# Performance work log

Hardware: AMD Instinct MI355X
Metric: run time of the kernel (lower is better)

Reference implementation:

```python
import jax, jax.numpy as jnp
import numpy as np

B, T, H, N, IN, W, D = 4096, 128, 64, 16, 32, 128, 8


def lipswish(x):
    return 0.909 * jax.nn.silu(x)


def setup_inputs() -> dict:
    key = jax.random.key(0)
    ks = jax.random.split(key, 10)

    def lin(k, i, o):
        kw, kb = jax.random.split(k)
        w = jax.random.normal(kw, (i, o), jnp.float32) / np.sqrt(i).astype(np.float32)
        b = jax.random.normal(kb, (o,), jnp.float32) * 0.01
        return w, b

    init_w0, init_b0 = lin(ks[0], IN, W)
    init_w1, init_b1 = lin(ks[1], W, H)
    drift_w0, drift_b0 = lin(ks[2], H + 1, W)
    drift_w1, drift_b1 = lin(ks[3], W, H)
    diff_w0, diff_b0 = lin(ks[4], H + 1, W)
    diff_w1, diff_b1 = lin(ks[5], W, H * N)
    ro_w, ro_b = lin(ks[6], H, D)
    ts = jnp.arange(T, dtype=jnp.float32)
    init_noise = jax.random.normal(ks[7], (B, IN), jnp.float32)
    # Brownian increments for unit steps: dW ~ N(0, dt) with dt = 1.
    dW = jax.random.normal(ks[8], (B, T - 1, N), jnp.float32)
    return dict(ts=ts, init_noise=init_noise, dW=dW,
                init_w0=init_w0, init_b0=init_b0, init_w1=init_w1, init_b1=init_b1,
                drift_w0=drift_w0, drift_b0=drift_b0, drift_w1=drift_w1, drift_b1=drift_b1,
                diff_w0=diff_w0, diff_b0=diff_b0, diff_w1=diff_w1, diff_b1=diff_b1,
                ro_w=ro_w, ro_b=ro_b)


def reference(ts, init_noise, dW,
              init_w0, init_b0, init_w1, init_b1,
              drift_w0, drift_b0, drift_w1, drift_b1,
              diff_w0, diff_b0, diff_w1, diff_b1,
              ro_w, ro_b):
    # initial MLP: default relu activation, identity final activation
    y0 = jnp.maximum(init_noise @ init_w0 + init_b0, 0.0) @ init_w1 + init_b1  # [B, H]

    def with_t(t, y):
        return jnp.concatenate([jnp.full((y.shape[0], 1), t, y.dtype), y], axis=1)

    def drift(t, y):  # [B, H]
        h = lipswish(with_t(t, y) @ drift_w0 + drift_b0)
        return jnp.tanh(h @ drift_w1 + drift_b1)

    def diffusion(t, y):  # [B, H, N]
        h = lipswish(with_t(t, y) @ diff_w0 + diff_b0)
        g = jnp.tanh(h @ diff_w1 + diff_b1)
        return g.reshape(y.shape[0], H, N)

    f0 = drift(ts[0], y0)
    g0 = diffusion(ts[0], y0)

    def step(carry, inp):
        y, yhat, f, g = carry
        t0, t1, dw = inp  # dw: [B, N]
        dt = t1 - t0
        # ReversibleHeun: yhat1 = 2 y - yhat + (f dt + g dW)
        yhat1 = 2.0 * y - yhat + f * dt + jnp.einsum('bhn,bn->bh', g, dw)
        f1 = drift(t1, yhat1)
        g1 = diffusion(t1, yhat1)
        y1 = y + 0.5 * ((f + f1) * dt + jnp.einsum('bhn,bn->bh', g + g1, dw))
        return (y1, yhat1, f1, g1), y1

    dWs = jnp.swapaxes(dW, 0, 1)  # [T-1, B, N]
    _, ys = jax.lax.scan(step, (y0, y0, f0, g0), (ts[:-1], ts[1:], dWs))
    ys = jnp.concatenate([y0[None], ys], axis=0)  # [T, B, H]
    out = jnp.einsum('tbh,hd->tbd', ys, ro_w) + ro_b
    return jnp.swapaxes(out, 0, 1)  # [B, T, D]
```

## Files before the change

### kernel.cpp

```cpp
#include <hip/hip_runtime.h>

#define NTHREADS 512
#define BB 8
#define SP 68


struct alignas(16) SMem {
    float dw0[65 * 128];
    float gw0[65 * 128];
    float db0[128];
    float db1[64];
    float gb0[128];
    float ro[512];
    float rob[8];
    float y[BB * SP];
    float yh[BB * SP];
    float f[BB * SP];
    float h[BB * 128];
    float dwn[BB * 16];
};

__device__ __forceinline__ float lipswish_f(float x) {
    const float e = expf(-x);
    const float d = __fadd_rn(1.0f, e);
    const float t = __fmul_rn(0.909f, x);
    return __fdiv_rn(t, d);
}

__global__ __launch_bounds__(NTHREADS, 4)
void sde_kernel(const float* __restrict__ ts, const float* __restrict__ init_noise,
                const float* __restrict__ dWin,
                const float* __restrict__ iw0, const float* __restrict__ ib0,
                const float* __restrict__ iw1, const float* __restrict__ ib1,
                const float* __restrict__ dr_w0, const float* __restrict__ dr_b0,
                const float* __restrict__ dr_w1, const float* __restrict__ dr_b1,
                const float* __restrict__ di_w0, const float* __restrict__ di_b0,
                const float* __restrict__ di_w1, const float* __restrict__ di_b1,
                const float* __restrict__ ro_w, const float* __restrict__ ro_b,
                float* __restrict__ out)
{
    __shared__ SMem sm;
    const int tid  = threadIdx.x;
    const int lane = tid & 63;
    const int wv   = tid >> 6;
    const int cg   = wv & 3;
    const int rg   = wv >> 2;
    const int b0   = blockIdx.x * BB;
    const int c0   = cg * 256 + (lane << 2);

    for (int i = tid; i < 65 * 128; i += NTHREADS) {
        sm.dw0[i] = dr_w0[i];
        sm.gw0[i] = di_w0[i];
    }
    if (tid < 128) sm.db0[tid] = dr_b0[tid];
    if (tid < 64)  sm.db1[tid] = dr_b1[tid];
    if (tid < 128) sm.gb0[tid] = di_b0[tid];
    if (tid < 512) sm.ro[tid] = ro_w[tid];
    if (tid < 8) sm.rob[tid] = ro_b[tid];

    float gb1v[4];
    {
        const float4 bv = *(const float4*)&di_b1[c0];
        gb1v[0] = bv.x; gb1v[1] = bv.y; gb1v[2] = bv.z; gb1v[3] = bv.w;
    }

    for (int i = tid; i < BB * 32; i += NTHREADS)
        sm.f[i] = init_noise[(size_t)(b0 + (i >> 5)) * 32 + (i & 31)];
    __syncthreads();

    {
        const int j = tid & 127, bq = tid >> 7;
        float acc[2];
        const float bj = ib0[j];
#pragma unroll
        for (int bi = 0; bi < 2; ++bi) acc[bi] = bj;
        for (int i = 0; i < 32; ++i) {
            const float w = iw0[i * 128 + j];
#pragma unroll
            for (int bi = 0; bi < 2; ++bi)
                acc[bi] = __fmaf_rn(sm.f[(bq * 2 + bi) * 32 + i], w, acc[bi]);
        }
#pragma unroll
        for (int bi = 0; bi < 2; ++bi)
            sm.h[(bq * 2 + bi) * 128 + j] = fmaxf(acc[bi], 0.0f);
    }
    __syncthreads();
    {
        const int hh = tid & 63, bg = tid >> 6;
        float acc = ib1[hh];
        for (int k = 0; k < 128; ++k)
            acc = __fmaf_rn(sm.h[bg * 128 + k], iw1[k * 64 + hh], acc);
        sm.y[bg * SP + hh]  = acc;
        sm.yh[bg * SP + hh] = acc;
    }
    __syncthreads();

    auto readout = [&](int trow) {
        if (tid < 64) {
            const int b = tid >> 3, d = tid & 7;
            float acc = sm.rob[d];
#pragma unroll
            for (int hh = 0; hh < 64; ++hh)
                acc = __fmaf_rn(sm.y[b * SP + hh], sm.ro[hh * 8 + d], acc);
            out[((size_t)(b0 + b) * 128 + trow) * 8 + d] = acc;
        }
    };
    readout(0);

    float g[4][4];

    auto layer1 = [&](const float* w0s, const float* b0s, float t1f) {
        const int j = tid & 127, bq = tid >> 7;
        float acc[2];
        const float bj = b0s[j];
        const float wt = w0s[j];
#pragma unroll
        for (int bi = 0; bi < 2; ++bi) acc[bi] = __fmaf_rn(t1f, wt, bj);
#pragma unroll 4
        for (int i = 0; i < 64; i += 4) {
            const float w0_ = w0s[(1 + i) * 128 + j];
            const float w1_ = w0s[(2 + i) * 128 + j];
            const float w2_ = w0s[(3 + i) * 128 + j];
            const float w3_ = w0s[(4 + i) * 128 + j];
#pragma unroll
            for (int bi = 0; bi < 2; ++bi) {
                const float4 xv = *(const float4*)&sm.yh[(bq * 2 + bi) * SP + i];
                acc[bi] = __fmaf_rn(xv.x, w0_, acc[bi]);
                acc[bi] = __fmaf_rn(xv.y, w1_, acc[bi]);
                acc[bi] = __fmaf_rn(xv.z, w2_, acc[bi]);
                acc[bi] = __fmaf_rn(xv.w, w3_, acc[bi]);
            }
        }
#pragma unroll
        for (int bi = 0; bi < 2; ++bi)
            sm.h[(bq * 2 + bi) * 128 + j] = lipswish_f(acc[bi]);
    };

    auto ein_bfly = [&](const float v[4], int b) -> float {
        float part = 0.0f;
#pragma unroll
        for (int e = 0; e < 4; ++e)
            part = __fmaf_rn(v[e], sm.dwn[b * 16 + (lane & 3) * 4 + e], part);
        part = __fadd_rn(part, __shfl_xor(part, 1, 64));
        part = __fadd_rn(part, __shfl_xor(part, 2, 64));
        return part;
    };

    auto mlp = [&](float t1f, float dtf, bool upd) {
        layer1(sm.dw0, sm.db0, t1f);
        __syncthreads();
        {
            const int hh = tid & 63, bg = tid >> 6;
            float acc = sm.db1[hh];
#pragma unroll 4
            for (int k = 0; k < 128; ++k)
                acc = __fmaf_rn(sm.h[bg * 128 + k], dr_w1[k * 64 + hh], acc);
            sm.f[bg * SP + hh] = tanhf(acc);
        }
        __syncthreads();
        layer1(sm.gw0, sm.gb0, t1f);
        __syncthreads();
        {
            float acc[4][4];
#pragma unroll
            for (int bi = 0; bi < 4; ++bi)
#pragma unroll
                for (int e = 0; e < 4; ++e) acc[bi][e] = 0.0f;

            float4 wA[4], wB[4], hA[4], hB[4];
#pragma unroll
            for (int t = 0; t < 4; ++t)
                wA[t] = *(const float4*)&di_w1[(size_t)t * 1024 + c0];
#pragma unroll
            for (int bi = 0; bi < 4; ++bi)
                hA[bi] = *(const float4*)&sm.h[(rg * 4 + bi) * 128];

#pragma unroll 1
            for (int kb = 0; kb < 128; kb += 8) {
                const int k2 = kb + 4;
#pragma unroll
                for (int t = 0; t < 4; ++t)
                    wB[t] = *(const float4*)&di_w1[(size_t)(k2 + t) * 1024 + c0];
#pragma unroll
                for (int bi = 0; bi < 4; ++bi)
                    hB[bi] = *(const float4*)&sm.h[(rg * 4 + bi) * 128 + k2];
#pragma unroll
                for (int bi = 0; bi < 4; ++bi) {
                    acc[bi][0] = __fmaf_rn(hA[bi].x, wA[0].x, acc[bi][0]);
                    acc[bi][1] = __fmaf_rn(hA[bi].x, wA[0].y, acc[bi][1]);
                    acc[bi][2] = __fmaf_rn(hA[bi].x, wA[0].z, acc[bi][2]);
                    acc[bi][3] = __fmaf_rn(hA[bi].x, wA[0].w, acc[bi][3]);
                    acc[bi][0] = __fmaf_rn(hA[bi].y, wA[1].x, acc[bi][0]);
                    acc[bi][1] = __fmaf_rn(hA[bi].y, wA[1].y, acc[bi][1]);
                    acc[bi][2] = __fmaf_rn(hA[bi].y, wA[1].z, acc[bi][2]);
                    acc[bi][3] = __fmaf_rn(hA[bi].y, wA[1].w, acc[bi][3]);
                    acc[bi][0] = __fmaf_rn(hA[bi].z, wA[2].x, acc[bi][0]);
                    acc[bi][1] = __fmaf_rn(hA[bi].z, wA[2].y, acc[bi][1]);
                    acc[bi][2] = __fmaf_rn(hA[bi].z, wA[2].z, acc[bi][2]);
                    acc[bi][3] = __fmaf_rn(hA[bi].z, wA[2].w, acc[bi][3]);
                    acc[bi][0] = __fmaf_rn(hA[bi].w, wA[3].x, acc[bi][0]);
                    acc[bi][1] = __fmaf_rn(hA[bi].w, wA[3].y, acc[bi][1]);
                    acc[bi][2] = __fmaf_rn(hA[bi].w, wA[3].z, acc[bi][2]);
                    acc[bi][3] = __fmaf_rn(hA[bi].w, wA[3].w, acc[bi][3]);
                }
                const int k3 = (kb + 8) & 127;
#pragma unroll
                for (int t = 0; t < 4; ++t)
                    wA[t] = *(const float4*)&di_w1[(size_t)(k3 + t) * 1024 + c0];
#pragma unroll
                for (int bi = 0; bi < 4; ++bi)
                    hA[bi] = *(const float4*)&sm.h[(rg * 4 + bi) * 128 + k3];
#pragma unroll
                for (int bi = 0; bi < 4; ++bi) {
                    acc[bi][0] = __fmaf_rn(hB[bi].x, wB[0].x, acc[bi][0]);
                    acc[bi][1] = __fmaf_rn(hB[bi].x, wB[0].y, acc[bi][1]);
                    acc[bi][2] = __fmaf_rn(hB[bi].x, wB[0].z, acc[bi][2]);
                    acc[bi][3] = __fmaf_rn(hB[bi].x, wB[0].w, acc[bi][3]);
                    acc[bi][0] = __fmaf_rn(hB[bi].y, wB[1].x, acc[bi][0]);
                    acc[bi][1] = __fmaf_rn(hB[bi].y, wB[1].y, acc[bi][1]);
                    acc[bi][2] = __fmaf_rn(hB[bi].y, wB[1].z, acc[bi][2]);
                    acc[bi][3] = __fmaf_rn(hB[bi].y, wB[1].w, acc[bi][3]);
                    acc[bi][0] = __fmaf_rn(hB[bi].z, wB[2].x, acc[bi][0]);
                    acc[bi][1] = __fmaf_rn(hB[bi].z, wB[2].y, acc[bi][1]);
                    acc[bi][2] = __fmaf_rn(hB[bi].z, wB[2].z, acc[bi][2]);
                    acc[bi][3] = __fmaf_rn(hB[bi].z, wB[2].w, acc[bi][3]);
                    acc[bi][0] = __fmaf_rn(hB[bi].w, wB[3].x, acc[bi][0]);
                    acc[bi][1] = __fmaf_rn(hB[bi].w, wB[3].y, acc[bi][1]);
                    acc[bi][2] = __fmaf_rn(hB[bi].w, wB[3].z, acc[bi][2]);
                    acc[bi][3] = __fmaf_rn(hB[bi].w, wB[3].w, acc[bi][3]);
                }
            }

#pragma unroll
            for (int bi = 0; bi < 4; ++bi) {
                const int b = rg * 4 + bi;
                float gv4[4];
#pragma unroll
                for (int e = 0; e < 4; ++e) {
                    const float gv = tanhf(__fadd_rn(acc[bi][e], gb1v[e]));
                    gv4[e] = gv;
                    g[bi][e] = gv;
                }
                if (upd) {
                    const float ein2 = ein_bfly(gv4, b);
                    if ((lane & 3) == 0) {
                        const int hh  = cg * 16 + (lane >> 2);
                        const int idx = b * SP + hh;
                        const float tot = __fmaf_rn(dtf, sm.f[idx], ein2);
                        sm.y[idx] = __fmaf_rn(0.5f, tot, sm.y[idx]);
                    }
                }
            }
        }
        __syncthreads();
    };

    mlp(ts[0], 0.0f, false);

    for (int s = 0; s < 127; ++s) {
        const float t1f = ts[s + 1];
        const float dtf = __fsub_rn(t1f, ts[s]);

        if (tid < BB * 16)
            sm.dwn[tid] = dWin[((size_t)(b0 + (tid >> 4)) * 127 + s) * 16 + (tid & 15)];
        __syncthreads();

#pragma unroll
        for (int bi = 0; bi < 4; ++bi) {
            const int b = rg * 4 + bi;
            const float ein1 = ein_bfly(g[bi], b);
            if ((lane & 3) == 0) {
                const int hh  = cg * 16 + (lane >> 2);
                const int idx = b * SP + hh;
                const float yv  = sm.y[idx];
                const float yhv = sm.yh[idx];
                const float inc = __fmaf_rn(dtf, sm.f[idx], ein1);
                const float a1  = __fmaf_rn(2.0f, yv, -yhv);
                sm.yh[idx] = __fadd_rn(a1, inc);
                sm.y[idx]  = __fmaf_rn(0.5f, inc, yv);
            }
        }
        __syncthreads();

        mlp(t1f, dtf, true);
        readout(s + 1);
    }
}

extern "C" void kernel_launch(void* const* d_in, const int* in_sizes, int n_in,
                              void* d_out, int out_size, void* d_ws, size_t ws_size,
                              hipStream_t stream) {
    (void)in_sizes; (void)n_in; (void)d_ws; (void)ws_size; (void)out_size;
    const float* ts         = (const float*)d_in[0];
    const float* init_noise = (const float*)d_in[1];
    const float* dW         = (const float*)d_in[2];
    const float* iw0        = (const float*)d_in[3];
    const float* ib0        = (const float*)d_in[4];
    const float* iw1        = (const float*)d_in[5];
    const float* ib1        = (const float*)d_in[6];
    const float* dr_w0      = (const float*)d_in[7];
    const float* dr_b0      = (const float*)d_in[8];
    const float* dr_w1      = (const float*)d_in[9];
    const float* dr_b1      = (const float*)d_in[10];
    const float* di_w0      = (const float*)d_in[11];
    const float* di_b0      = (const float*)d_in[12];
    const float* di_w1      = (const float*)d_in[13];
    const float* di_b1      = (const float*)d_in[14];
    const float* ro_w       = (const float*)d_in[15];
    const float* ro_b       = (const float*)d_in[16];
    float* out = (float*)d_out;

    sde_kernel<<<dim3(4096 / BB), dim3(NTHREADS), 0, stream>>>(
        ts, init_noise, dW, iw0, ib0, iw1, ib1,
        dr_w0, dr_b0, dr_w1, dr_b1, di_w0, di_b0, di_w1, di_b1,
        ro_w, ro_b, out);
}
```

Baseline: 3.745 ms.

## Fuse drift and diffusion MLP layers, keep state in registers, cut barriers

Computes the drift and diffusion first layers in one pass over yhat, and folds the drift second layer into the diffusion second-layer GEMM loop. Per-thread state (y, yhat, f, midpoint) now lives in registers, and f is shared within each 4-lane group by shuffles. dW is prefetched one step ahead into registers instead of staged through shared memory. This cuts the barriers per step from about six to three and removes the separate f and readout shared buffers. In exchange, register pressure rises at 4 blocks per CU, and the readout now reads weights straight from global memory.

```diff
diff --git a/kernel.cpp b/kernel.cpp
--- a/kernel.cpp
+++ b/kernel.cpp
@@ -11,13 +11,10 @@
     float db0[128];
     float db1[64];
     float gb0[128];
-    float ro[512];
-    float rob[8];
-    float y[BB * SP];
+    float y [BB * SP];
     float yh[BB * SP];
-    float f[BB * SP];
-    float h[BB * 128];
-    float dwn[BB * 16];
+    float hd[BB * 128];
+    float hg[BB * 128];
 };
 
 __device__ __forceinline__ float lipswish_f(float x) {
@@ -47,6 +44,10 @@
     const int rg   = wv >> 2;
     const int b0   = blockIdx.x * BB;
     const int c0   = cg * 256 + (lane << 2);
+    const int q    = lane & 3;
+    const int hh_own = cg * 16 + (lane >> 2);
+    const int rb   = rg * 4 + q;
+    const bool owner = (q == 0);
 
     for (int i = tid; i < 65 * 128; i += NTHREADS) {
         sm.dw0[i] = dr_w0[i];
@@ -55,8 +56,6 @@
     if (tid < 128) sm.db0[tid] = dr_b0[tid];
     if (tid < 64)  sm.db1[tid] = dr_b1[tid];
     if (tid < 128) sm.gb0[tid] = di_b0[tid];
-    if (tid < 512) sm.ro[tid] = ro_w[tid];
-    if (tid < 8) sm.rob[tid] = ro_b[tid];
 
     float gb1v[4];
     {
@@ -65,7 +64,7 @@
     }
 
     for (int i = tid; i < BB * 32; i += NTHREADS)
-        sm.f[i] = init_noise[(size_t)(b0 + (i >> 5)) * 32 + (i & 31)];
+        sm.hg[i] = init_noise[(size_t)(b0 + (i >> 5)) * 32 + (i & 31)];
     __syncthreads();
 
     {
@@ -78,213 +77,248 @@
             const float w = iw0[i * 128 + j];
 #pragma unroll
             for (int bi = 0; bi < 2; ++bi)
-                acc[bi] = __fmaf_rn(sm.f[(bq * 2 + bi) * 32 + i], w, acc[bi]);
+                acc[bi] = __fmaf_rn(sm.hg[(bq * 2 + bi) * 32 + i], w, acc[bi]);
         }
 #pragma unroll
         for (int bi = 0; bi < 2; ++bi)
-            sm.h[(bq * 2 + bi) * 128 + j] = fmaxf(acc[bi], 0.0f);
+            sm.hd[(bq * 2 + bi) * 128 + j] = fmaxf(acc[bi], 0.0f);
     }
     __syncthreads();
     {
         const int hh = tid & 63, bg = tid >> 6;
         float acc = ib1[hh];
         for (int k = 0; k < 128; ++k)
-            acc = __fmaf_rn(sm.h[bg * 128 + k], iw1[k * 64 + hh], acc);
+            acc = __fmaf_rn(sm.hd[bg * 128 + k], iw1[k * 64 + hh], acc);
         sm.y[bg * SP + hh]  = acc;
         sm.yh[bg * SP + hh] = acc;
     }
     __syncthreads();
 
     auto readout = [&](int trow) {
-        if (tid < 64) {
-            const int b = tid >> 3, d = tid & 7;
-            float acc = sm.rob[d];
-#pragma unroll
-            for (int hh = 0; hh < 64; ++hh)
-                acc = __fmaf_rn(sm.y[b * SP + hh], sm.ro[hh * 8 + d], acc);
-            out[((size_t)(b0 + b) * 128 + trow) * 8 + d] = acc;
-        }
+        const int b = tid >> 3, d = tid & 7;
+        float acc = ro_b[d];
+#pragma unroll
+        for (int hh = 0; hh < 64; ++hh)
+            acc = __fmaf_rn(sm.y[b * SP + hh], ro_w[hh * 8 + d], acc);
+        out[((size_t)(b0 + b) * 128 + trow) * 8 + d] = acc;
     };
-    readout(0);
-
+
+    float y4[4], yh4[4], ymid4[4], f4[4];
     float g[4][4];
-
-    auto layer1 = [&](const float* w0s, const float* b0s, float t1f) {
-        const int j = tid & 127, bq = tid >> 7;
-        float acc[2];
-        const float bj = b0s[j];
-        const float wt = w0s[j];
-#pragma unroll
-        for (int bi = 0; bi < 2; ++bi) acc[bi] = __fmaf_rn(t1f, wt, bj);
-#pragma unroll 4
-        for (int i = 0; i < 64; i += 4) {
-            const float w0_ = w0s[(1 + i) * 128 + j];
-            const float w1_ = w0s[(2 + i) * 128 + j];
-            const float w2_ = w0s[(3 + i) * 128 + j];
-            const float w3_ = w0s[(4 + i) * 128 + j];
-#pragma unroll
-            for (int bi = 0; bi < 2; ++bi) {
-                const float4 xv = *(const float4*)&sm.yh[(bq * 2 + bi) * SP + i];
-                acc[bi] = __fmaf_rn(xv.x, w0_, acc[bi]);
-                acc[bi] = __fmaf_rn(xv.y, w1_, acc[bi]);
-                acc[bi] = __fmaf_rn(xv.z, w2_, acc[bi]);
-                acc[bi] = __fmaf_rn(xv.w, w3_, acc[bi]);
-            }
-        }
-#pragma unroll
-        for (int bi = 0; bi < 2; ++bi)
-            sm.h[(bq * 2 + bi) * 128 + j] = lipswish_f(acc[bi]);
-    };
-
-    auto ein_bfly = [&](const float v[4], int b) -> float {
+    float4 dwC[4], dwN[4];
+
+#pragma unroll
+    for (int bi = 0; bi < 4; ++bi) {
+        const float v = sm.y[(rg * 4 + bi) * SP + hh_own];
+        y4[bi] = v; yh4[bi] = v;
+        dwC[bi] = *(const float4*)&dWin[((size_t)(b0 + rg * 4 + bi) * 127 + 0) * 16 + q * 4];
+        ymid4[bi] = 0.0f; f4[bi] = 0.0f;
+    }
+
+    auto ein_bfly = [&](const float v[4], const float4 dw) -> float {
         float part = 0.0f;
-#pragma unroll
-        for (int e = 0; e < 4; ++e)
-            part = __fmaf_rn(v[e], sm.dwn[b * 16 + (lane & 3) * 4 + e], part);
+        part = __fmaf_rn(v[0], dw.x, part);
+        part = __fmaf_rn(v[1], dw.y, part);
+        part = __fmaf_rn(v[2], dw.z, part);
+        part = __fmaf_rn(v[3], dw.w, part);
         part = __fadd_rn(part, __shfl_xor(part, 1, 64));
         part = __fadd_rn(part, __shfl_xor(part, 2, 64));
         return part;
     };
 
-    auto mlp = [&](float t1f, float dtf, bool upd) {
-        layer1(sm.dw0, sm.db0, t1f);
-        __syncthreads();
+    auto layer12 = [&](float t1f) {
+        const int j = tid & 127, bq = tid >> 7;
+        float aD[2], aG[2];
         {
-            const int hh = tid & 63, bg = tid >> 6;
-            float acc = sm.db1[hh];
+            const float bD = sm.db0[j], wtD = sm.dw0[j];
+            const float bG = sm.gb0[j], wtG = sm.gw0[j];
+#pragma unroll
+            for (int bi = 0; bi < 2; ++bi) {
+                aD[bi] = __fmaf_rn(t1f, wtD, bD);
+                aG[bi] = __fmaf_rn(t1f, wtG, bG);
+            }
+        }
 #pragma unroll 4
-            for (int k = 0; k < 128; ++k)
-                acc = __fmaf_rn(sm.h[bg * 128 + k], dr_w1[k * 64 + hh], acc);
-            sm.f[bg * SP + hh] = tanhf(acc);
-        }
-        __syncthreads();
-        layer1(sm.gw0, sm.gb0, t1f);
-        __syncthreads();
-        {
-            float acc[4][4];
+        for (int i = 0; i < 64; i += 4) {
+            const float wD0 = sm.dw0[(1 + i) * 128 + j];
+            const float wD1 = sm.dw0[(2 + i) * 128 + j];
+            const float wD2 = sm.dw0[(3 + i) * 128 + j];
+            const float wD3 = sm.dw0[(4 + i) * 128 + j];
+            const float wG0 = sm.gw0[(1 + i) * 128 + j];
+            const float wG1 = sm.gw0[(2 + i) * 128 + j];
+            const float wG2 = sm.gw0[(3 + i) * 128 + j];
+            const float wG3 = sm.gw0[(4 + i) * 128 + j];
+#pragma unroll
+            for (int bi = 0; bi < 2; ++bi) {
+                const float4 xv = *(const float4*)&sm.yh[(bq * 2 + bi) * SP + i];
+                aD[bi] = __fmaf_rn(xv.x, wD0, aD[bi]);
+                aD[bi] = __fmaf_rn(xv.y, wD1, aD[bi]);
+                aD[bi] = __fmaf_rn(xv.z, wD2, aD[bi]);
+                aD[bi] = __fmaf_rn(xv.w, wD3, aD[bi]);
+                aG[bi] = __fmaf_rn(xv.x, wG0, aG[bi]);
+                aG[bi] = __fmaf_rn(xv.y, wG1, aG[bi]);
+                aG[bi] = __fmaf_rn(xv.z, wG2, aG[bi]);
+                aG[bi] = __fmaf_rn(xv.w, wG3, aG[bi]);
+            }
+        }
+#pragma unroll
+        for (int bi = 0; bi < 2; ++bi) {
+            sm.hd[(bq * 2 + bi) * 128 + j] = lipswish_f(aD[bi]);
+            sm.hg[(bq * 2 + bi) * 128 + j] = lipswish_f(aG[bi]);
+        }
+    };
+
+    auto gf_phase = [&](float dtf, bool upd) {
+        float acc[4][4];
+#pragma unroll
+        for (int bi = 0; bi < 4; ++bi)
+#pragma unroll
+            for (int e = 0; e < 4; ++e) acc[bi][e] = 0.0f;
+        float fa = sm.db1[hh_own];
+
+        float4 wA[4], wB[4], hA[4], hB[4];
+#pragma unroll
+        for (int t = 0; t < 4; ++t)
+            wA[t] = *(const float4*)&di_w1[(size_t)t * 1024 + c0];
+#pragma unroll
+        for (int bi = 0; bi < 4; ++bi)
+            hA[bi] = *(const float4*)&sm.hg[(rg * 4 + bi) * 128];
+
+#pragma unroll 1
+        for (int kb = 0; kb < 128; kb += 8) {
+            const int k2 = kb + 4;
+            const float fw0 = dr_w1[(kb + 0) * 64 + hh_own];
+            const float fw1 = dr_w1[(kb + 1) * 64 + hh_own];
+            const float fw2 = dr_w1[(kb + 2) * 64 + hh_own];
+            const float fw3 = dr_w1[(kb + 3) * 64 + hh_own];
+            const float fw4 = dr_w1[(kb + 4) * 64 + hh_own];
+            const float fw5 = dr_w1[(kb + 5) * 64 + hh_own];
+            const float fw6 = dr_w1[(kb + 6) * 64 + hh_own];
+            const float fw7 = dr_w1[(kb + 7) * 64 + hh_own];
+#pragma unroll
+            for (int t = 0; t < 4; ++t)
+                wB[t] = *(const float4*)&di_w1[(size_t)(k2 + t) * 1024 + c0];
 #pragma unroll
             for (int bi = 0; bi < 4; ++bi)
-#pragma unroll
-                for (int e = 0; e < 4; ++e) acc[bi][e] = 0.0f;
-
-            float4 wA[4], wB[4], hA[4], hB[4];
+                hB[bi] = *(const float4*)&sm.hg[(rg * 4 + bi) * 128 + k2];
+#pragma unroll
+            for (int bi = 0; bi < 4; ++bi) {
+                acc[bi][0] = __fmaf_rn(hA[bi].x, wA[0].x, acc[bi][0]);
+                acc[bi][1] = __fmaf_rn(hA[bi].x, wA[0].y, acc[bi][1]);
+                acc[bi][2] = __fmaf_rn(hA[bi].x, wA[0].z, acc[bi][2]);
+                acc[bi][3] = __fmaf_rn(hA[bi].x, wA[0].w, acc[bi][3]);
+                acc[bi][0] = __fmaf_rn(hA[bi].y, wA[1].x, acc[bi][0]);
+                acc[bi][1] = __fmaf_rn(hA[bi].y, wA[1].y, acc[bi][1]);
+                acc[bi][2] = __fmaf_rn(hA[bi].y, wA[1].z, acc[bi][2]);
+                acc[bi][3] = __fmaf_rn(hA[bi].y, wA[1].w, acc[bi][3]);
+                acc[bi][0] = __fmaf_rn(hA[bi].z, wA[2].x, acc[bi][0]);
+                acc[bi][1] = __fmaf_rn(hA[bi].z, wA[2].y, acc[bi][1]);
+                acc[bi][2] = __fmaf_rn(hA[bi].z, wA[2].z, acc[bi][2]);
+                acc[bi][3] = __fmaf_rn(hA[bi].z, wA[2].w, acc[bi][3]);
+                acc[bi][0] = __fmaf_rn(hA[bi].w, wA[3].x, acc[bi][0]);
+                acc[bi][1] = __fmaf_rn(hA[bi].w, wA[3].y, acc[bi][1]);
+                acc[bi][2] = __fmaf_rn(hA[bi].w, wA[3].z, acc[bi][2]);
+                acc[bi][3] = __fmaf_rn(hA[bi].w, wA[3].w, acc[bi][3]);
+            }
+            const int k3 = (kb + 8) & 127;
 #pragma unroll
             for (int t = 0; t < 4; ++t)
-                wA[t] = *(const float4*)&di_w1[(size_t)t * 1024 + c0];
+                wA[t] = *(const float4*)&di_w1[(size_t)(k3 + t) * 1024 + c0];
 #pragma unroll
             for (int bi = 0; bi < 4; ++bi)
-                hA[bi] = *(const float4*)&sm.h[(rg * 4 + bi) * 128];
-
-#pragma unroll 1
-            for (int kb = 0; kb < 128; kb += 8) {
-                const int k2 = kb + 4;
-#pragma unroll
-                for (int t = 0; t < 4; ++t)
-                    wB[t] = *(const float4*)&di_w1[(size_t)(k2 + t) * 1024 + c0];
-#pragma unroll
-                for (int bi = 0; bi < 4; ++bi)
-                    hB[bi] = *(const float4*)&sm.h[(rg * 4 + bi) * 128 + k2];
-#pragma unroll
-                for (int bi = 0; bi < 4; ++bi) {
-                    acc[bi][0] = __fmaf_rn(hA[bi].x, wA[0].x, acc[bi][0]);
-                    acc[bi][1] = __fmaf_rn(hA[bi].x, wA[0].y, acc[bi][1]);
-                    acc[bi][2] = __fmaf_rn(hA[bi].x, wA[0].z, acc[bi][2]);
-                    acc[bi][3] = __fmaf_rn(hA[bi].x, wA[0].w, acc[bi][3]);
-                    acc[bi][0] = __fmaf_rn(hA[bi].y, wA[1].x, acc[bi][0]);
-                    acc[bi][1] = __fmaf_rn(hA[bi].y, wA[1].y, acc[bi][1]);
-                    acc[bi][2] = __fmaf_rn(hA[bi].y, wA[1].z, acc[bi][2]);
-                    acc[bi][3] = __fmaf_rn(hA[bi].y, wA[1].w, acc[bi][3]);
-                    acc[bi][0] = __fmaf_rn(hA[bi].z, wA[2].x, acc[bi][0]);
-                    acc[bi][1] = __fmaf_rn(hA[bi].z, wA[2].y, acc[bi][1]);
-                    acc[bi][2] = __fmaf_rn(hA[bi].z, wA[2].z, acc[bi][2]);
-                    acc[bi][3] = __fmaf_rn(hA[bi].z, wA[2].w, acc[bi][3]);
-                    acc[bi][0] = __fmaf_rn(hA[bi].w, wA[3].x, acc[bi][0]);
-                    acc[bi][1] = __fmaf_rn(hA[bi].w, wA[3].y, acc[bi][1]);
-                    acc[bi][2] = __fmaf_rn(hA[bi].w, wA[3].z, acc[bi][2]);
-                    acc[bi][3] = __fmaf_rn(hA[bi].w, wA[3].w, acc[bi][3]);
+                hA[bi] = *(const float4*)&sm.hg[(rg * 4 + bi) * 128 + k3];
+#pragma unroll
+            for (int bi = 0; bi < 4; ++bi) {
+                acc[bi][0] = __fmaf_rn(hB[bi].x, wB[0].x, acc[bi][0]);
+                acc[bi][1] = __fmaf_rn(hB[bi].x, wB[0].y, acc[bi][1]);
+                acc[bi][2] = __fmaf_rn(hB[bi].x, wB[0].z, acc[bi][2]);
+                acc[bi][3] = __fmaf_rn(hB[bi].x, wB[0].w, acc[bi][3]);
+                acc[bi][0] = __fmaf_rn(hB[bi].y, wB[1].x, acc[bi][0]);
+                acc[bi][1] = __fmaf_rn(hB[bi].y, wB[1].y, acc[bi][1]);
+                acc[bi][2] = __fmaf_rn(hB[bi].y, wB[1].z, acc[bi][2]);
+                acc[bi][3] = __fmaf_rn(hB[bi].y, wB[1].w, acc[bi][3]);
+                acc[bi][0] = __fmaf_rn(hB[bi].z, wB[2].x, acc[bi][0]);
+                acc[bi][1] = __fmaf_rn(hB[bi].z, wB[2].y, acc[bi][1]);
+                acc[bi][2] = __fmaf_rn(hB[bi].z, wB[2].z, acc[bi][2]);
+                acc[bi][3] = __fmaf_rn(hB[bi].z, wB[2].w, acc[bi][3]);
+                acc[bi][0] = __fmaf_rn(hB[bi].w, wB[3].x, acc[bi][0]);
+                acc[bi][1] = __fmaf_rn(hB[bi].w, wB[3].y, acc[bi][1]);
+                acc[bi][2] = __fmaf_rn(hB[bi].w, wB[3].z, acc[bi][2]);
+                acc[bi][3] = __fmaf_rn(hB[bi].w, wB[3].w, acc[bi][3]);
+            }
+            fa = __fmaf_rn(sm.hd[rb * 128 + kb + 0], fw0, fa);
+            fa = __fmaf_rn(sm.hd[rb * 128 + kb + 1], fw1, fa);
+            fa = __fmaf_rn(sm.hd[rb * 128 + kb + 2], fw2, fa);
+            fa = __fmaf_rn(sm.hd[rb * 128 + kb + 3], fw3, fa);
+            fa = __fmaf_rn(sm.hd[rb * 128 + kb + 4], fw4, fa);
+            fa = __fmaf_rn(sm.hd[rb * 128 + kb + 5], fw5, fa);
+            fa = __fmaf_rn(sm.hd[rb * 128 + kb + 6], fw6, fa);
+            fa = __fmaf_rn(sm.hd[rb * 128 + kb + 7], fw7, fa);
+        }
+
+        const float fv = tanhf(fa);
+#pragma unroll
+        for (int bi = 0; bi < 4; ++bi)
+            f4[bi] = __shfl(fv, (lane & ~3) + bi, 64);
+
+#pragma unroll
+        for (int bi = 0; bi < 4; ++bi) {
+            float gv4[4];
+#pragma unroll
+            for (int e = 0; e < 4; ++e) {
+                const float gv = tanhf(__fadd_rn(acc[bi][e], gb1v[e]));
+                gv4[e] = gv;
+                g[bi][e] = gv;
+            }
+            if (upd) {
+                const float ein2 = ein_bfly(gv4, dwC[bi]);
+                if (owner) {
+                    const float tot = __fmaf_rn(dtf, f4[bi], ein2);
+                    const float yn  = __fmaf_rn(0.5f, tot, ymid4[bi]);
+                    sm.y[(rg * 4 + bi) * SP + hh_own] = yn;
+                    y4[bi] = yn;
                 }
-                const int k3 = (kb + 8) & 127;
-#pragma unroll
-                for (int t = 0; t < 4; ++t)
-                    wA[t] = *(const float4*)&di_w1[(size_t)(k3 + t) * 1024 + c0];
-#pragma unroll
-                for (int bi = 0; bi < 4; ++bi)
-                    hA[bi] = *(const float4*)&sm.h[(rg * 4 + bi) * 128 + k3];
-#pragma unroll
-                for (int bi = 0; bi < 4; ++bi) {
-                    acc[bi][0] = __fmaf_rn(hB[bi].x, wB[0].x, acc[bi][0]);
-                    acc[bi][1] = __fmaf_rn(hB[bi].x, wB[0].y, acc[bi][1]);
-                    acc[bi][2] = __fmaf_rn(hB[bi].x, wB[0].z, acc[bi][2]);
-                    acc[bi][3] = __fmaf_rn(hB[bi].x, wB[0].w, acc[bi][3]);
-                    acc[bi][0] = __fmaf_rn(hB[bi].y, wB[1].x, acc[bi][0]);
-                    acc[bi][1] = __fmaf_rn(hB[bi].y, wB[1].y, acc[bi][1]);
-                    acc[bi][2] = __fmaf_rn(hB[bi].y, wB[1].z, acc[bi][2]);
-                    acc[bi][3] = __fmaf_rn(hB[bi].y, wB[1].w, acc[bi][3]);
-                    acc[bi][0] = __fmaf_rn(hB[bi].z, wB[2].x, acc[bi][0]);
-                    acc[bi][1] = __fmaf_rn(hB[bi].z, wB[2].y, acc[bi][1]);
-                    acc[bi][2] = __fmaf_rn(hB[bi].z, wB[2].z, acc[bi][2]);
-                    acc[bi][3] = __fmaf_rn(hB[bi].z, wB[2].w, acc[bi][3]);
-                    acc[bi][0] = __fmaf_rn(hB[bi].w, wB[3].x, acc[bi][0]);
-                    acc[bi][1] = __fmaf_rn(hB[bi].w, wB[3].y, acc[bi][1]);
-                    acc[bi][2] = __fmaf_rn(hB[bi].w, wB[3].z, acc[bi][2]);
-                    acc[bi][3] = __fmaf_rn(hB[bi].w, wB[3].w, acc[bi][3]);
-                }
-            }
-
-#pragma unroll
-            for (int bi = 0; bi < 4; ++bi) {
-                const int b = rg * 4 + bi;
-                float gv4[4];
-#pragma unroll
-                for (int e = 0; e < 4; ++e) {
-                    const float gv = tanhf(__fadd_rn(acc[bi][e], gb1v[e]));
-                    gv4[e] = gv;
-                    g[bi][e] = gv;
-                }
-                if (upd) {
-                    const float ein2 = ein_bfly(gv4, b);
-                    if ((lane & 3) == 0) {
-                        const int hh  = cg * 16 + (lane >> 2);
-                        const int idx = b * SP + hh;
-                        const float tot = __fmaf_rn(dtf, sm.f[idx], ein2);
-                        sm.y[idx] = __fmaf_rn(0.5f, tot, sm.y[idx]);
-                    }
-                }
-            }
-        }
-        __syncthreads();
+            }
+        }
     };
 
-    mlp(ts[0], 0.0f, false);
+    layer12(ts[0]);
+    __syncthreads();
+    gf_phase(0.0f, false);
+    __syncthreads();
 
     for (int s = 0; s < 127; ++s) {
         const float t1f = ts[s + 1];
         const float dtf = __fsub_rn(t1f, ts[s]);
 
-        if (tid < BB * 16)
-            sm.dwn[tid] = dWin[((size_t)(b0 + (tid >> 4)) * 127 + s) * 16 + (tid & 15)];
+        if (tid < 64) readout(s);
+#pragma unroll
+        for (int bi = 0; bi < 4; ++bi) {
+            const float ein1 = ein_bfly(g[bi], dwC[bi]);
+            if (owner) {
+                const float inc = __fmaf_rn(dtf, f4[bi], ein1);
+                const float a1  = __fmaf_rn(2.0f, y4[bi], -yh4[bi]);
+                const float yhn = __fadd_rn(a1, inc);
+                sm.yh[(rg * 4 + bi) * SP + hh_own] = yhn;
+                yh4[bi]   = yhn;
+                ymid4[bi] = __fmaf_rn(0.5f, inc, y4[bi]);
+            }
+        }
         __syncthreads();
 
-#pragma unroll
-        for (int bi = 0; bi < 4; ++bi) {
-            const int b = rg * 4 + bi;
-            const float ein1 = ein_bfly(g[bi], b);
-            if ((lane & 3) == 0) {
-                const int hh  = cg * 16 + (lane >> 2);
-                const int idx = b * SP + hh;
-                const float yv  = sm.y[idx];
-                const float yhv = sm.yh[idx];
-                const float inc = __fmaf_rn(dtf, sm.f[idx], ein1);
-                const float a1  = __fmaf_rn(2.0f, yv, -yhv);
-                sm.yh[idx] = __fadd_rn(a1, inc);
-                sm.y[idx]  = __fmaf_rn(0.5f, inc, yv);
-            }
-        }
+        const int sn = (s < 126) ? (s + 1) : 126;
+#pragma unroll
+        for (int bi = 0; bi < 4; ++bi)
+            dwN[bi] = *(const float4*)&dWin[((size_t)(b0 + rg * 4 + bi) * 127 + sn) * 16 + q * 4];
+        layer12(t1f);
         __syncthreads();
 
-        mlp(t1f, dtf, true);
-        readout(s + 1);
-    }
+        gf_phase(dtf, true);
+#pragma unroll
+        for (int bi = 0; bi < 4; ++bi) dwC[bi] = dwN[bi];
+        __syncthreads();
+    }
+    if (tid < 64) readout(127);
 }
 
 extern "C" void kernel_launch(void* const* d_in, const int* in_sizes, int n_in,
```

New measurement: 5.186 ms. 1.38x slower.

## Remap diffusion GEMM thread tiling and pad hidden buffer to avoid bank conflicts

Applied to the files above, without the earlier changes.

Pads the shared hidden-activation rows to a stride of 132 floats so per-row float4 reads fall in different LDS banks. Remaps the diffusion output-layer tiling so each wave covers 128 contiguous output columns and the lanes alternate between two groups of four batch rows, instead of four column groups by two row groups. The einsum butterfly reduction, the owner-lane predicate and the drift second-layer thread mapping are changed to match the new lane layout. The aim is fewer LDS bank conflicts and better locality of the global weight loads, at the cost of more intricate index arithmetic.

```diff
diff --git a/kernel.cpp b/kernel.cpp
--- a/kernel.cpp
+++ b/kernel.cpp
@@ -3,6 +3,7 @@
 #define NTHREADS 512
 #define BB 8
 #define SP 68
+#define SH 132
 
 
 struct alignas(16) SMem {
@@ -16,7 +17,7 @@
     float y[BB * SP];
     float yh[BB * SP];
     float f[BB * SP];
-    float h[BB * 128];
+    float h[BB * SH];
     float dwn[BB * 16];
 };
 
@@ -43,10 +44,17 @@
     const int tid  = threadIdx.x;
     const int lane = tid & 63;
     const int wv   = tid >> 6;
-    const int cg   = wv & 3;
-    const int rg   = wv >> 2;
     const int b0   = blockIdx.x * BB;
-    const int c0   = cg * 256 + (lane << 2);
+
+    const int r    = lane & 1;
+    const int qn   = (lane >> 1) & 3;
+    const int a    = lane >> 3;
+    const int c0   = wv * 128 + (lane >> 1) * 4;
+    const int rb0  = r * 4;
+    const int hh_own = wv * 8 + a;
+    const bool owner = ((lane & 6) == 0);
+    const int fb = lane >> 3;
+    const int fc = wv * 8 + (lane & 7);
 
     for (int i = tid; i < 65 * 128; i += NTHREADS) {
         sm.dw0[i] = dr_w0[i];
@@ -82,14 +90,14 @@
         }
 #pragma unroll
         for (int bi = 0; bi < 2; ++bi)
-            sm.h[(bq * 2 + bi) * 128 + j] = fmaxf(acc[bi], 0.0f);
+            sm.h[(bq * 2 + bi) * SH + j] = fmaxf(acc[bi], 0.0f);
     }
     __syncthreads();
     {
         const int hh = tid & 63, bg = tid >> 6;
         float acc = ib1[hh];
         for (int k = 0; k < 128; ++k)
-            acc = __fmaf_rn(sm.h[bg * 128 + k], iw1[k * 64 + hh], acc);
+            acc = __fmaf_rn(sm.h[bg * SH + k], iw1[k * 64 + hh], acc);
         sm.y[bg * SP + hh]  = acc;
         sm.yh[bg * SP + hh] = acc;
     }
@@ -133,16 +141,16 @@
         }
 #pragma unroll
         for (int bi = 0; bi < 2; ++bi)
-            sm.h[(bq * 2 + bi) * 128 + j] = lipswish_f(acc[bi]);
+            sm.h[(bq * 2 + bi) * SH + j] = lipswish_f(acc[bi]);
     };
 
     auto ein_bfly = [&](const float v[4], int b) -> float {
         float part = 0.0f;
 #pragma unroll
         for (int e = 0; e < 4; ++e)
-            part = __fmaf_rn(v[e], sm.dwn[b * 16 + (lane & 3) * 4 + e], part);
-        part = __fadd_rn(part, __shfl_xor(part, 1, 64));
+            part = __fmaf_rn(v[e], sm.dwn[b * 16 + qn * 4 + e], part);
         part = __fadd_rn(part, __shfl_xor(part, 2, 64));
+        part = __fadd_rn(part, __shfl_xor(part, 4, 64));
         return part;
     };
 
@@ -150,12 +158,11 @@
         layer1(sm.dw0, sm.db0, t1f);
         __syncthreads();
         {
-            const int hh = tid & 63, bg = tid >> 6;
-            float acc = sm.db1[hh];
+            float acc = sm.db1[fc];
 #pragma unroll 4
             for (int k = 0; k < 128; ++k)
-                acc = __fmaf_rn(sm.h[bg * 128 + k], dr_w1[k * 64 + hh], acc);
-            sm.f[bg * SP + hh] = tanhf(acc);
+                acc = __fmaf_rn(sm.h[fb * SH + k], dr_w1[k * 64 + fc], acc);
+            sm.f[fb * SP + fc] = tanhf(acc);
         }
         __syncthreads();
         layer1(sm.gw0, sm.gb0, t1f);
@@ -173,7 +180,7 @@
                 wA[t] = *(const float4*)&di_w1[(size_t)t * 1024 + c0];
 #pragma unroll
             for (int bi = 0; bi < 4; ++bi)
-                hA[bi] = *(const float4*)&sm.h[(rg * 4 + bi) * 128];
+                hA[bi] = *(const float4*)&sm.h[(rb0 + bi) * SH];
 
 #pragma unroll 1
             for (int kb = 0; kb < 128; kb += 8) {
@@ -183,7 +190,7 @@
                     wB[t] = *(const float4*)&di_w1[(size_t)(k2 + t) * 1024 + c0];
 #pragma unroll
                 for (int bi = 0; bi < 4; ++bi)
-                    hB[bi] = *(const float4*)&sm.h[(rg * 4 + bi) * 128 + k2];
+                    hB[bi] = *(const float4*)&sm.h[(rb0 + bi) * SH + k2];
 #pragma unroll
                 for (int bi = 0; bi < 4; ++bi) {
                     acc[bi][0] = __fmaf_rn(hA[bi].x, wA[0].x, acc[bi][0]);
@@ -209,7 +216,7 @@
                     wA[t] = *(const float4*)&di_w1[(size_t)(k3 + t) * 1024 + c0];
 #pragma unroll
                 for (int bi = 0; bi < 4; ++bi)
-                    hA[bi] = *(const float4*)&sm.h[(rg * 4 + bi) * 128 + k3];
+                    hA[bi] = *(const float4*)&sm.h[(rb0 + bi) * SH + k3];
 #pragma unroll
                 for (int bi = 0; bi < 4; ++bi) {
                     acc[bi][0] = __fmaf_rn(hB[bi].x, wB[0].x, acc[bi][0]);
@@ -233,7 +240,7 @@
 
 #pragma unroll
             for (int bi = 0; bi < 4; ++bi) {
-                const int b = rg * 4 + bi;
+                const int b = rb0 + bi;
                 float gv4[4];
 #pragma unroll
                 for (int e = 0; e < 4; ++e) {
@@ -243,9 +250,8 @@
                 }
                 if (upd) {
                     const float ein2 = ein_bfly(gv4, b);
-                    if ((lane & 3) == 0) {
-                        const int hh  = cg * 16 + (lane >> 2);
-                        const int idx = b * SP + hh;
+                    if (owner) {
+                        const int idx = b * SP + hh_own;
                         const float tot = __fmaf_rn(dtf, sm.f[idx], ein2);
                         sm.y[idx] = __fmaf_rn(0.5f, tot, sm.y[idx]);
                     }
@@ -267,11 +273,10 @@
 
 #pragma unroll
         for (int bi = 0; bi < 4; ++bi) {
-            const int b = rg * 4 + bi;
+            const int b = rb0 + bi;
             const float ein1 = ein_bfly(g[bi], b);
-            if ((lane & 3) == 0) {
-                const int hh  = cg * 16 + (lane >> 2);
-                const int idx = b * SP + hh;
+            if (owner) {
+                const int idx = b * SP + hh_own;
                 const float yv  = sm.y[idx];
                 const float yhv = sm.yh[idx];
                 const float inc = __fmaf_rn(dtf, sm.f[idx], ein1);
```

After: 3.762 ms. About the same (+0.5%).
